# Performance work log

Measured on AMD Instinct MI355X. Metric: run time of the kernel, lower is better.

The kernel has to match this reference:

```python
import jax, jax.numpy as jnp
import numpy as np

E, H, FF, L, S, B = 64, 4, 32, 9, 7, 8192
HD = E // H


def setup_inputs() -> dict:
    key = jax.random.key(0)
    ks = iter(jax.random.split(key, 32))
    def rn(shape, scale=0.05):
        return jax.random.normal(next(ks), shape, dtype=jnp.float32) * scale
    inp = {
        "feature1": jax.random.normal(next(ks), (B, S, E), dtype=jnp.float32),
        "feature2": jax.random.normal(next(ks), (B, S, E), dtype=jnp.float32),
        # branch dim 2: index 0 = rotation, 1 = translation; then layer dim L
        "sa1_win": rn((2, L, 3 * E, E)), "sa1_bin": rn((2, L, 3 * E)),
        "sa1_wout": rn((2, L, E, E)), "sa1_bout": rn((2, L, E)),
        "sa2_win": rn((2, L, 3 * E, E)), "sa2_bin": rn((2, L, 3 * E)),
        "sa2_wout": rn((2, L, E, E)), "sa2_bout": rn((2, L, E)),
        "ca_win": rn((2, L, 3 * E, E)), "ca_bin": rn((2, L, 3 * E)),
        "ca_wout": rn((2, L, E, E)), "ca_bout": rn((2, L, E)),
        "ff_w1": rn((2, L, FF, E)), "ff_b1": rn((2, L, FF)),
        "ff_w2": rn((2, L, E, FF)), "ff_b2": rn((2, L, E)),
        "query_embed": jax.random.normal(next(ks), (2, S, E), dtype=jnp.float32),
        "fc_rot_w": rn((4, E)), "fc_rot_b": rn((4,)),
        "fc_trans_w": rn((3, E)), "fc_trans_b": rn((3,)),
    }
    return inp


def mha(q_in, kv_in, win, b_in, wout, bout):
    # torch nn.MultiheadAttention with batch_first=True
    wq, wk, wv = win[:E], win[E:2 * E], win[2 * E:]
    bq, bk, bv = b_in[:E], b_in[E:2 * E], b_in[2 * E:]
    b, sq, _ = q_in.shape
    sk = kv_in.shape[1]
    q = (q_in @ wq.T + bq).reshape(b, sq, H, HD)
    k = (kv_in @ wk.T + bk).reshape(b, sk, H, HD)
    v = (kv_in @ wv.T + bv).reshape(b, sk, H, HD)
    scores = jnp.einsum("bqhd,bkhd->bhqk", q, k) / jnp.sqrt(jnp.float32(HD))
    attn = jax.nn.softmax(scores, axis=-1)
    ctx = jnp.einsum("bhqk,bkhd->bqhd", attn, v).reshape(b, sq, E)
    return ctx @ wout.T + bout


def _branch(f1, f2, query, bi, sa1_win, sa1_bin, sa1_wout, sa1_bout,
            sa2_win, sa2_bin, sa2_wout, sa2_bout,
            ca_win, ca_bin, ca_wout, ca_bout, ff_w1, ff_b1, ff_w2, ff_b2):
    q = query
    for i in range(L):
        f1 = f1 + mha(f1, f1, sa1_win[bi, i], sa1_bin[bi, i], sa1_wout[bi, i], sa1_bout[bi, i])
        f2 = f2 + mha(f2, f2, sa2_win[bi, i], sa2_bin[bi, i], sa2_wout[bi, i], sa2_bout[bi, i])
        kv = jnp.concatenate([f1, f2], axis=1)  # (B, 2S, E)
        q = q + mha(q, kv, ca_win[bi, i], ca_bin[bi, i], ca_wout[bi, i], ca_bout[bi, i])
        h = jax.nn.relu(q @ ff_w1[bi, i].T + ff_b1[bi, i])
        q = q + h @ ff_w2[bi, i].T + ff_b2[bi, i]
    return q


def reference(feature1, feature2, sa1_win, sa1_bin, sa1_wout, sa1_bout,
              sa2_win, sa2_bin, sa2_wout, sa2_bout,
              ca_win, ca_bin, ca_wout, ca_bout,
              ff_w1, ff_b1, ff_w2, ff_b2, query_embed,
              fc_rot_w, fc_rot_b, fc_trans_w, fc_trans_b):
    b = feature1.shape[0]
    args = (sa1_win, sa1_bin, sa1_wout, sa1_bout, sa2_win, sa2_bin, sa2_wout,
            sa2_bout, ca_win, ca_bin, ca_wout, ca_bout, ff_w1, ff_b1, ff_w2, ff_b2)
    q_rot = jnp.broadcast_to(query_embed[0][None], (b, S, E))
    q_trn = jnp.broadcast_to(query_embed[1][None], (b, S, E))
    # rotation and translation branches are mathematically independent
    rot = _branch(feature1, feature2, q_rot, 0, *args)
    trn = _branch(feature1, feature2, q_trn, 1, *args)
    pose_rot = (rot @ fc_rot_w.T + fc_rot_b).mean(axis=1)    # (B, 4)
    pose_trn = (trn @ fc_trans_w.T + fc_trans_b).mean(axis=1)  # (B, 3)
    return jnp.concatenate([pose_rot, pose_trn], axis=1)  # (B, 7)
```

## Files before the change

kernel.cpp:

```cpp
#include <hip/hip_runtime.h>
#include <hip/hip_bf16.h>

namespace {

using bf16x8 = __attribute__((ext_vector_type(8))) short;
using f32x4  = __attribute__((ext_vector_type(4))) float;

constexpr int NL = 9, S = 7, BB = 8192;
constexpr int G = 8;
constexpr int M = G * S;
constexpr int NT = 512;

constexpr int OFF_F1 = 0;
constexpr int OFF_F2 = 14336;
constexpr int OFF_Q  = 28672;
constexpr int OFF_QB = 43008;
constexpr int OFF_KB = 50176;
constexpr int OFF_VT = 64512;
constexpr int SMEM_TOTAL = 80896;

__device__ __forceinline__ unsigned short f2bf(float f) {
  union { __hip_bfloat16 h; unsigned short s; } u;
  u.h = __float2bfloat16(f);
  return u.s;
}
__device__ __forceinline__ uint32_t pk2(float a, float b) {
  return (uint32_t)f2bf(a) | ((uint32_t)f2bf(b) << 16);
}
__device__ __forceinline__ int swzS(int r, int c) {
  return r * 256 + ((((c >> 3) ^ (r & 7)) << 5) | ((c & 7) << 2));
}
__device__ __forceinline__ int swzB(int r, int c) {
  return r * 128 + ((((c >> 3) ^ (r & 7)) << 4) | ((c & 7) << 1));
}
__device__ __forceinline__ int swzV(int d, int kv) {
  return d * 256 + ((((kv >> 3) ^ (d & 7)) << 4) | ((kv & 7) << 1));
}
__device__ __forceinline__ int div7(int t) { return (t * 9363) >> 16; }

__device__ __forceinline__ bf16x8 ldStateFrag(const char* base, int r, int k0) {
  const float4* p = (const float4*)(base + r * 256 + (((k0 >> 3) ^ (r & 7)) << 5));
  float4 x = p[0], y = p[1];
  union { bf16x8 v; uint32_t u[4]; } o;
  o.u[0] = pk2(x.x, x.y); o.u[1] = pk2(x.z, x.w);
  o.u[2] = pk2(y.x, y.y); o.u[3] = pk2(y.z, y.w);
  return o.v;
}
__device__ __forceinline__ bf16x8 ldBfFrag(const char* base, int r, int k0) {
  return *(const bf16x8*)(base + r * 128 + (((k0 >> 3) ^ (r & 7)) << 4));
}

template <int MTOT, int NTOT, int KF, int WMG, int WNG, int VNT, bool WS,
          class BLD, class STN, class STV>
__device__ __forceinline__ void gemm_sw(const short* __restrict__ wbf,
                                        const float* __restrict__ wf,
                                        const float* __restrict__ bias,
                                        int ldK, int wid, int lane,
                                        BLD bld, STN stn, STV stv)
{
  const int wm = wid / WNG, wn = wid % WNG;
  const int q = lane & 15, gI = lane >> 4;
  constexpr int MPW = (MTOT + WMG - 1) / WMG;
  constexpr int NPW = NTOT / WNG;
  bf16x8 bfr[MPW][KF];
#pragma unroll
  for (int i = 0; i < MPW; ++i) {
    const int mt = wm * MPW + i;
    if (mt < MTOT) {
#pragma unroll
      for (int kf = 0; kf < KF; ++kf)
        bfr[i][kf] = bld(mt * 16 + q, kf * 32 + gI * 8);
    }
  }
#pragma unroll
  for (int j = 0; j < NPW; ++j) {
    const int nt = wn * NPW + j;
    bf16x8 afr[KF];
#pragma unroll
    for (int kf = 0; kf < KF; ++kf) {
      const int k0 = kf * 32 + gI * 8;
      if constexpr (WS) {
        afr[kf] = *(const bf16x8*)(wbf + (size_t)(nt * 16 + q) * ldK + k0);
      } else {
        const float* wp = wf + (size_t)(nt * 16 + q) * ldK + k0;
        float4 x = *(const float4*)wp, y = *(const float4*)(wp + 4);
        union { bf16x8 v; uint32_t u[4]; } o;
        o.u[0] = pk2(x.x, x.y); o.u[1] = pk2(x.z, x.w);
        o.u[2] = pk2(y.x, y.y); o.u[3] = pk2(y.z, y.w);
        afr[kf] = o.v;
      }
    }
    if (nt < VNT) {
      const float4 b4 = *(const float4*)(bias + nt * 16 + gI * 4);
#pragma unroll
      for (int i = 0; i < MPW; ++i) {
        const int mt = wm * MPW + i;
        if (mt < MTOT) {
          f32x4 acc = { b4.x, b4.y, b4.z, b4.w };
#pragma unroll
          for (int kf = 0; kf < KF; ++kf)
            acc = __builtin_amdgcn_mfma_f32_16x16x32_bf16(afr[kf], bfr[i][kf], acc, 0, 0, 0);
          stn(mt, nt, acc);
        }
      }
    } else {
      const float bv = bias[nt * 16 + q];
#pragma unroll
      for (int i = 0; i < MPW; ++i) {
        const int mt = wm * MPW + i;
        if (mt < MTOT) {
          f32x4 acc = { bv, bv, bv, bv };
#pragma unroll
          for (int kf = 0; kf < KF; ++kf)
            acc = __builtin_amdgcn_mfma_f32_16x16x32_bf16(bfr[i][kf], afr[kf], acc, 0, 0, 0);
          stv(mt, nt, acc);
        }
      }
    }
  }
}

template <bool CA_>
__device__ __forceinline__ void attn(char* qb, const char* kb, const char* vt,
                                     int wid, int lane)
{
  const int q = lane & 15, gI = lane >> 4;
  const int g = wid;
  constexpr int KVL = CA_ ? 14 : 7;
#pragma unroll
  for (int h = 0; h < 4; ++h) {
    bf16x8 kfrag = {}, qfrag = {};
    if (gI < 2) {
      int qrow = g * 7 + q; qrow = qrow > 55 ? 55 : qrow;
      qfrag = ldBfFrag(qb, qrow, h * 16 + gI * 8);
      int kvr;
      if constexpr (CA_) {
        kvr = (q < 7) ? (g * 7 + q) : (49 + g * 7 + q);
        kvr = kvr > 111 ? 111 : kvr;
      } else {
        kvr = g * 7 + q; kvr = kvr > 55 ? 55 : kvr;
      }
      kfrag = ldBfFrag(kb, kvr, h * 16 + gI * 8);
    }
    f32x4 s = { 0.f, 0.f, 0.f, 0.f };
    s = __builtin_amdgcn_mfma_f32_16x16x32_bf16(kfrag, qfrag, s, 0, 0, 0);

    float e[4]; float sum = 0.f;
#pragma unroll
    for (int jj = 0; jj < 4; ++jj) {
      const int kvloc = gI * 4 + jj;
      const float tt = fminf(s[jj] * 0.36067376f, 60.f);
      e[jj] = (kvloc < KVL) ? exp2f(tt) : 0.f;
      sum += e[jj];
    }
    sum += __shfl_xor(sum, 16);
    sum += __shfl_xor(sum, 32);
    const float inv = __builtin_amdgcn_rcpf(sum);

    union { bf16x8 v; uint32_t u[4]; } pb;
    pb.u[0] = pk2(e[0] * inv, e[1] * inv);
    pb.u[1] = pk2(e[2] * inv, e[3] * inv);
    pb.u[2] = 0; pb.u[3] = 0;

    const int d = h * 16 + q;
    const int kv0 = (CA_ ? g * 16 : g * 8) + gI * 4;
    const uint2 vv = *(const uint2*)(vt + swzV(d, kv0));
    union { bf16x8 v; uint32_t u[4]; } va;
    va.u[0] = vv.x; va.u[1] = vv.y; va.u[2] = 0; va.u[3] = 0;

    f32x4 o = { 0.f, 0.f, 0.f, 0.f };
    o = __builtin_amdgcn_mfma_f32_16x16x32_bf16(va.v, pb.v, o, 0, 0, 0);

    if (q < 7) {
      const int tok = g * 7 + q, c0 = h * 16 + gI * 4;
      *(uint2*)(qb + swzB(tok, c0)) = make_uint2(pk2(o[0], o[1]), pk2(o[2], o[3]));
    }
  }
}

template <bool WS>
__global__ __launch_bounds__(NT, 4) void pose_kernel(
    const float* __restrict__ feature1, const float* __restrict__ feature2,
    const float* __restrict__ sa1_win, const float* __restrict__ sa1_bin,
    const float* __restrict__ sa1_wout, const float* __restrict__ sa1_bout,
    const float* __restrict__ sa2_win, const float* __restrict__ sa2_bin,
    const float* __restrict__ sa2_wout, const float* __restrict__ sa2_bout,
    const float* __restrict__ ca_win, const float* __restrict__ ca_bin,
    const float* __restrict__ ca_wout, const float* __restrict__ ca_bout,
    const float* __restrict__ ff_w1, const float* __restrict__ ff_b1,
    const float* __restrict__ ff_w2, const float* __restrict__ ff_b2,
    const float* __restrict__ query_embed,
    const float* __restrict__ fc_rot_w, const float* __restrict__ fc_rot_b,
    const float* __restrict__ fc_trans_w, const float* __restrict__ fc_trans_b,
    const short* __restrict__ wbf, float* __restrict__ out)
{
  extern __shared__ char smem[];
  char* sF1 = smem + OFF_F1;
  char* sF2 = smem + OFF_F2;
  char* sQ  = smem + OFF_Q;
  char* qb  = smem + OFF_QB;
  char* kb  = smem + OFF_KB;
  char* vt  = smem + OFF_VT;

  const int t = threadIdx.x;
  const int wid = t >> 6, lane = t & 63;
  const int q = lane & 15, gI = lane >> 4;
  const int bi = blockIdx.y;
  const int b0 = blockIdx.x * G;

  {
    const uint4 z = { 0, 0, 0, 0 };
    for (int i = t; i < 1024; i += NT) ((uint4*)vt)[i] = z;
  }
  {
    const float* f1p = feature1 + (size_t)b0 * (S * 64);
    const float* f2p = feature2 + (size_t)b0 * (S * 64);
    const float* qe  = query_embed + (size_t)bi * (S * 64);
    for (int idx = t; idx < M * 64; idx += NT) {
      const int r = idx >> 6, c = idx & 63;
      const int s = r - div7(r) * 7;
      *(float*)(sF1 + swzS(r, c)) = f1p[idx];
      *(float*)(sF2 + swzS(r, c)) = f2p[idx];
      *(float*)(sQ + swzS(r, c))  = qe[s * 64 + c];
    }
  }
  __syncthreads();

  const auto stv_none = [](int, int, f32x4) {};

  for (int li = 0; li < NL; ++li) {
    const int wo = bi * NL + li;
    const short* W_in[3]  = { wbf + 0      + wo * 12288,
                              wbf + 221184 + wo * 12288,
                              wbf + 442368 + wo * 12288 };
    const short* W_out[3] = { wbf + 663552 + wo * 4096,
                              wbf + 737280 + wo * 4096,
                              wbf + 811008 + wo * 4096 };
    const short* W_f1 = wbf + 884736 + wo * 2048;
    const short* W_f2 = wbf + 921600 + wo * 2048;
    const float* F_in[3]  = { sa1_win + wo * 12288, sa2_win + wo * 12288, ca_win + wo * 12288 };
    const float* F_out[3] = { sa1_wout + wo * 4096, sa2_wout + wo * 4096, ca_wout + wo * 4096 };
    const float* B_in[3]  = { sa1_bin + wo * 192, sa2_bin + wo * 192, ca_bin + wo * 192 };
    const float* B_out[3] = { sa1_bout + wo * 64, sa2_bout + wo * 64, ca_bout + wo * 64 };

    for (int sa = 0; sa < 2; ++sa) {
      char* ST = sa ? sF2 : sF1;
      auto bld = [&](int r, int k0) { return ldStateFrag(ST, r > 55 ? 55 : r, k0); };
      auto stn = [&](int mt, int nt, f32x4 a) {
        const int tok = mt * 16 + q; if (tok >= M) return;
        if (nt < 4) {
          *(uint2*)(qb + swzB(tok, nt * 16 + gI * 4)) =
              make_uint2(pk2(a[0], a[1]), pk2(a[2], a[3]));
        } else {
          *(uint2*)(kb + swzB(tok, (nt - 4) * 16 + gI * 4)) =
              make_uint2(pk2(a[0], a[1]), pk2(a[2], a[3]));
        }
      };
      auto stv = [&](int mt, int nt, f32x4 a) {
        const int d = (nt - 8) * 16 + q;
#pragma unroll
        for (int jj = 0; jj < 4; ++jj) {
          const int tok = mt * 16 + gI * 4 + jj;
          if (tok < M) {
            const int g = div7(tok);
            *(short*)(vt + swzV(d, g * 8 + (tok - g * 7))) = (short)f2bf(a[jj]);
          }
        }
      };
      gemm_sw<4, 12, 2, 2, 4, 8, WS>(W_in[sa], F_in[sa], B_in[sa], 64, wid, lane, bld, stn, stv);
      __syncthreads();
      attn<false>(qb, kb, vt, wid, lane);
      __syncthreads();
      auto bldc = [&](int r, int k0) { return ldBfFrag(qb, r > 55 ? 55 : r, k0); };
      auto stres = [&](int mt, int nt, f32x4 a) {
        const int tok = mt * 16 + q; if (tok >= M) return;
        const int c0 = nt * 16 + gI * 4;
        float4* p = (float4*)(ST + tok * 256 + (((c0 >> 3) ^ (tok & 7)) << 5) + (c0 & 7) * 4);
        float4 v = *p;
        v.x += a[0]; v.y += a[1]; v.z += a[2]; v.w += a[3];
        *p = v;
      };
      gemm_sw<4, 4, 2, 2, 4, 4, WS>(W_out[sa], F_out[sa], B_out[sa], 64, wid, lane, bldc, stres, stv_none);
      __syncthreads();
    }

    {
      auto bldq = [&](int r, int k0) { return ldStateFrag(sQ, r > 55 ? 55 : r, k0); };
      auto stq = [&](int mt, int nt, f32x4 a) {
        const int tok = mt * 16 + q; if (tok >= M) return;
        *(uint2*)(qb + swzB(tok, nt * 16 + gI * 4)) =
            make_uint2(pk2(a[0], a[1]), pk2(a[2], a[3]));
      };
      gemm_sw<4, 4, 2, 2, 4, 4, WS>(W_in[2], F_in[2], B_in[2], 64, wid, lane, bldq, stq, stv_none);

      for (int src = 0; src < 2; ++src) {
        const char* SRC = src ? sF2 : sF1;
        auto bld = [&](int r, int k0) { return ldStateFrag(SRC, r > 55 ? 55 : r, k0); };
        auto stk = [&](int mt, int nt, f32x4 a) {
          const int tok = mt * 16 + q; if (tok >= M) return;
          *(uint2*)(kb + swzB(tok + src * 56, nt * 16 + gI * 4)) =
              make_uint2(pk2(a[0], a[1]), pk2(a[2], a[3]));
        };
        auto stv = [&](int mt, int nt, f32x4 a) {
          const int d = (nt - 4) * 16 + q;
#pragma unroll
          for (int jj = 0; jj < 4; ++jj) {
            const int tok = mt * 16 + gI * 4 + jj;
            if (tok < M) {
              const int g = div7(tok);
              *(short*)(vt + swzV(d, g * 16 + (tok - g * 7) + src * 7)) = (short)f2bf(a[jj]);
            }
          }
        };
        gemm_sw<4, 8, 2, 2, 4, 4, WS>(W_in[2] + 4096, F_in[2] + 4096, B_in[2] + 64,
                                      64, wid, lane, bld, stk, stv);
      }
      __syncthreads();
      attn<true>(qb, kb, vt, wid, lane);
      __syncthreads();
      auto bldc = [&](int r, int k0) { return ldBfFrag(qb, r > 55 ? 55 : r, k0); };
      auto stres = [&](int mt, int nt, f32x4 a) {
        const int tok = mt * 16 + q; if (tok >= M) return;
        const int c0 = nt * 16 + gI * 4;
        float4* p = (float4*)(sQ + tok * 256 + (((c0 >> 3) ^ (tok & 7)) << 5) + (c0 & 7) * 4);
        float4 v = *p;
        v.x += a[0]; v.y += a[1]; v.z += a[2]; v.w += a[3];
        *p = v;
      };
      gemm_sw<4, 4, 2, 2, 4, 4, WS>(W_out[2], F_out[2], B_out[2], 64, wid, lane, bldc, stres, stv_none);
      __syncthreads();
    }

    {
      auto bldq = [&](int r, int k0) { return ldStateFrag(sQ, r > 55 ? 55 : r, k0); };
      auto sth = [&](int mt, int nt, f32x4 a) {
        const int tok = mt * 16 + q; if (tok >= M) return;
        *(uint2*)(qb + swzB(tok, nt * 16 + gI * 4)) =
            make_uint2(pk2(fmaxf(a[0], 0.f), fmaxf(a[1], 0.f)),
                       pk2(fmaxf(a[2], 0.f), fmaxf(a[3], 0.f)));
      };
      gemm_sw<4, 2, 2, 4, 2, 2, WS>(W_f1, ff_w1 + wo * 2048, ff_b1 + wo * 32,
                                    64, wid, lane, bldq, sth, stv_none);
      __syncthreads();
      auto bldh = [&](int r, int k0) { return ldBfFrag(qb, r > 55 ? 55 : r, k0); };
      auto stres = [&](int mt, int nt, f32x4 a) {
        const int tok = mt * 16 + q; if (tok >= M) return;
        const int c0 = nt * 16 + gI * 4;
        float4* p = (float4*)(sQ + tok * 256 + (((c0 >> 3) ^ (tok & 7)) << 5) + (c0 & 7) * 4);
        float4 v = *p;
        v.x += a[0]; v.y += a[1]; v.z += a[2]; v.w += a[3];
        *p = v;
      };
      gemm_sw<4, 4, 1, 2, 4, 4, WS>(W_f2, ff_w2 + wo * 2048, ff_b2 + wo * 64,
                                    32, wid, lane, bldh, stres, stv_none);
      __syncthreads();
    }
  }

  float* cs = (float*)qb;
  {
    const int g = t >> 6, c = t & 63;
    float a = 0.f;
#pragma unroll
    for (int s = 0; s < 7; ++s) a += *(const float*)(sQ + swzS(g * 7 + s, c));
    cs[t] = a;
  }
  __syncthreads();
  const int ncols = bi ? 3 : 4;
  if (t < G * ncols) {
    const int g = t / ncols, cc = t - g * ncols;
    const float* wv = bi ? (fc_trans_w + cc * 64) : (fc_rot_w + cc * 64);
    float acc = 0.f;
#pragma unroll
    for (int k = 0; k < 64; ++k) acc += cs[g * 64 + k] * wv[k];
    const float bb = bi ? fc_trans_b[cc] : fc_rot_b[cc];
    out[(size_t)(b0 + g) * 7 + (bi ? 4 : 0) + cc] = acc * (1.f / 7.f) + bb;
  }
}

__global__ void prep_kernel(const float* __restrict__ a0, const float* __restrict__ a1,
                            const float* __restrict__ a2, const float* __restrict__ a3,
                            const float* __restrict__ a4, const float* __restrict__ a5,
                            const float* __restrict__ a6, const float* __restrict__ a7,
                            short* __restrict__ dst)
{
  for (int i = blockIdx.x * blockDim.x + threadIdx.x; i < 958464;
       i += gridDim.x * blockDim.x) {
    const float* s; int j;
    if      (i < 221184) { s = a0; j = i; }
    else if (i < 442368) { s = a1; j = i - 221184; }
    else if (i < 663552) { s = a2; j = i - 442368; }
    else if (i < 737280) { s = a3; j = i - 663552; }
    else if (i < 811008) { s = a4; j = i - 737280; }
    else if (i < 884736) { s = a5; j = i - 811008; }
    else if (i < 921600) { s = a6; j = i - 884736; }
    else                 { s = a7; j = i - 921600; }
    dst[i] = (short)f2bf(s[j]);
  }
}

}

extern "C" void kernel_launch(void* const* d_in, const int* in_sizes, int n_in,
                              void* d_out, int out_size, void* d_ws, size_t ws_size,
                              hipStream_t stream)
{
  const float* feature1    = (const float*)d_in[0];
  const float* feature2    = (const float*)d_in[1];
  const float* sa1_win     = (const float*)d_in[2];
  const float* sa1_bin     = (const float*)d_in[3];
  const float* sa1_wout    = (const float*)d_in[4];
  const float* sa1_bout    = (const float*)d_in[5];
  const float* sa2_win     = (const float*)d_in[6];
  const float* sa2_bin     = (const float*)d_in[7];
  const float* sa2_wout    = (const float*)d_in[8];
  const float* sa2_bout    = (const float*)d_in[9];
  const float* ca_win      = (const float*)d_in[10];
  const float* ca_bin      = (const float*)d_in[11];
  const float* ca_wout     = (const float*)d_in[12];
  const float* ca_bout     = (const float*)d_in[13];
  const float* ff_w1       = (const float*)d_in[14];
  const float* ff_b1       = (const float*)d_in[15];
  const float* ff_w2       = (const float*)d_in[16];
  const float* ff_b2       = (const float*)d_in[17];
  const float* query_embed = (const float*)d_in[18];
  const float* fc_rot_w    = (const float*)d_in[19];
  const float* fc_rot_b    = (const float*)d_in[20];
  const float* fc_trans_w  = (const float*)d_in[21];
  const float* fc_trans_b  = (const float*)d_in[22];

  const bool ws_ok = (d_ws != nullptr) && (ws_size >= (size_t)958464 * 2);
  dim3 grid(BB / G, 2);

  if (ws_ok) {
    prep_kernel<<<dim3(936), 512, 0, stream>>>(sa1_win, sa2_win, ca_win,
                                               sa1_wout, sa2_wout, ca_wout,
                                               ff_w1, ff_w2, (short*)d_ws);
    hipFuncSetAttribute(reinterpret_cast<const void*>(&pose_kernel<true>),
                        hipFuncAttributeMaxDynamicSharedMemorySize, SMEM_TOTAL);
    pose_kernel<true><<<grid, NT, SMEM_TOTAL, stream>>>(
        feature1, feature2,
        sa1_win, sa1_bin, sa1_wout, sa1_bout,
        sa2_win, sa2_bin, sa2_wout, sa2_bout,
        ca_win, ca_bin, ca_wout, ca_bout,
        ff_w1, ff_b1, ff_w2, ff_b2,
        query_embed, fc_rot_w, fc_rot_b, fc_trans_w, fc_trans_b,
        (const short*)d_ws, (float*)d_out);
  } else {
    hipFuncSetAttribute(reinterpret_cast<const void*>(&pose_kernel<false>),
                        hipFuncAttributeMaxDynamicSharedMemorySize, SMEM_TOTAL);
    pose_kernel<false><<<grid, NT, SMEM_TOTAL, stream>>>(
        feature1, feature2,
        sa1_win, sa1_bin, sa1_wout, sa1_bout,
        sa2_win, sa2_bin, sa2_wout, sa2_bout,
        ca_win, ca_bin, ca_wout, ca_bout,
        ff_w1, ff_b1, ff_w2, ff_b2,
        query_embed, fc_rot_w, fc_rot_b, fc_trans_w, fc_trans_b,
        (const short*)d_ws, (float*)d_out);
  }
}
```

Before: 1.301 ms.

## Pack 7 batches per block and merge self-attention stages to cut padding and barriers

Reduces the batch group per block from 8 to 7 so that 49 tokens pack tightly into 4 MFMA row tiles, down from 56 tokens, cutting wasted padding. Both self-attention branches now share one synchronisation phase: QKV projections run back to back, a single attention pass spreads 14 units over 8 waves, and the two output projections run together. The CA K/V projection handles F1 and F2 in one 98-row GEMM. Per-layer barriers drop, but the grid needs a partial last block with bounds checks, and the attention load across waves is uneven.

```diff
diff --git a/kernel.cpp b/kernel.cpp
--- a/kernel.cpp
+++ b/kernel.cpp
@@ -6,18 +6,18 @@
 using bf16x8 = __attribute__((ext_vector_type(8))) short;
 using f32x4  = __attribute__((ext_vector_type(4))) float;
 
-constexpr int NL = 9, S = 7, BB = 8192;
-constexpr int G = 8;
-constexpr int M = G * S;
+constexpr int NL = 9, BB = 8192;
+constexpr int G = 7;
+constexpr int M1 = 49;
 constexpr int NT = 512;
 
 constexpr int OFF_F1 = 0;
-constexpr int OFF_F2 = 14336;
-constexpr int OFF_Q  = 28672;
-constexpr int OFF_QB = 43008;
+constexpr int OFF_F2 = 12544;
+constexpr int OFF_SQ = 25088;
+constexpr int OFF_QB = 37632;
 constexpr int OFF_KB = 50176;
-constexpr int OFF_VT = 64512;
-constexpr int SMEM_TOTAL = 80896;
+constexpr int OFF_VT = 62720;
+constexpr int SMEM_TOTAL = 79104;
 
 __device__ __forceinline__ unsigned short f2bf(float f) {
   union { __hip_bfloat16 h; unsigned short s; } u;
@@ -50,26 +50,107 @@
   return *(const bf16x8*)(base + r * 128 + (((k0 >> 3) ^ (r & 7)) << 4));
 }
 
-template <int MTOT, int NTOT, int KF, int WMG, int WNG, int VNT, bool WS,
-          class BLD, class STN, class STV>
-__device__ __forceinline__ void gemm_sw(const short* __restrict__ wbf,
-                                        const float* __restrict__ wf,
-                                        const float* __restrict__ bias,
-                                        int ldK, int wid, int lane,
-                                        BLD bld, STN stn, STV stv)
+enum : int { BS_F1 = 0, BS_F2, BS_SQ, BS_F1F2, BS_QB0, BS_QB49 };
+
+template <int BS>
+__device__ __forceinline__ bf16x8 bfrag(const char* smem, int r, int k0)
+{
+  if constexpr (BS == BS_F1) {
+    return ldStateFrag(smem + OFF_F1, r > 48 ? 48 : r, k0);
+  } else if constexpr (BS == BS_F2) {
+    return ldStateFrag(smem + OFF_F2, r > 48 ? 48 : r, k0);
+  } else if constexpr (BS == BS_SQ) {
+    return ldStateFrag(smem + OFF_SQ, r > 48 ? 48 : r, k0);
+  } else if constexpr (BS == BS_F1F2) {
+    const int f2 = r >= 49;
+    int rr = f2 ? r - 49 : r;
+    rr = rr > 48 ? 48 : rr;
+    return ldStateFrag(smem + (f2 ? OFF_F2 : OFF_F1), rr, k0);
+  } else if constexpr (BS == BS_QB0) {
+    return ldBfFrag(smem + OFF_QB, r > 97 ? 97 : r, k0);
+  } else {
+    int rr = r > 48 ? 48 : r;
+    return ldBfFrag(smem + OFF_QB, 49 + rr, k0);
+  }
+}
+
+enum : int { OM_QKV0 = 0, OM_QKV1, OM_QCA, OM_KVCA, OM_RESF0, OM_RESF1, OM_RESQ, OM_RELU };
+
+template <int OM>
+__device__ __forceinline__ void epi_n(char* smem, int nt, int tok, int gI, f32x4 a)
+{
+  if constexpr (OM == OM_RESF0 || OM == OM_RESF1 || OM == OM_RESQ) {
+    constexpr int off = (OM == OM_RESF0) ? OFF_F1 : (OM == OM_RESF1) ? OFF_F2 : OFF_SQ;
+    const int c0 = nt * 16 + gI * 4;
+    float4* p = (float4*)(smem + off + tok * 256 + (((c0 >> 3) ^ (tok & 7)) << 5) + ((c0 & 7) << 2));
+    float4 v = *p;
+    v.x += a[0]; v.y += a[1]; v.z += a[2]; v.w += a[3];
+    *p = v;
+  } else if constexpr (OM == OM_RELU) {
+    *(uint2*)(smem + OFF_QB + swzB(tok, nt * 16 + gI * 4)) =
+        make_uint2(pk2(fmaxf(a[0], 0.f), fmaxf(a[1], 0.f)),
+                   pk2(fmaxf(a[2], 0.f), fmaxf(a[3], 0.f)));
+  } else {
+    const uint2 val = make_uint2(pk2(a[0], a[1]), pk2(a[2], a[3]));
+    if constexpr (OM == OM_QKV0 || OM == OM_QKV1) {
+      constexpr int RO = (OM == OM_QKV1) ? 49 : 0;
+      if (nt < 4) *(uint2*)(smem + OFF_QB + swzB(RO + tok, nt * 16 + gI * 4)) = val;
+      else        *(uint2*)(smem + OFF_KB + swzB(RO + tok, (nt - 4) * 16 + gI * 4)) = val;
+    } else if constexpr (OM == OM_QCA) {
+      *(uint2*)(smem + OFF_QB + swzB(tok, nt * 16 + gI * 4)) = val;
+    } else {
+      const int f2 = tok >= 49;
+      const int t2 = f2 ? tok - 49 : tok;
+      const int g = div7(t2);
+      const int row = 14 * g + (t2 - 7 * g) + (f2 ? 7 : 0);
+      *(uint2*)(smem + OFF_KB + swzB(row, nt * 16 + gI * 4)) = val;
+    }
+  }
+}
+
+template <int OM>
+__device__ __forceinline__ void epi_v(char* smem, int d, int tokbase, f32x4 a)
+{
+#pragma unroll
+  for (int jj = 0; jj < 4; ++jj) {
+    const int tok = tokbase + jj;
+    if constexpr (OM == OM_QKV0 || OM == OM_QKV1) {
+      if (tok < 49) {
+        const int g = div7(tok);
+        const int slot = ((OM == OM_QKV1) ? 56 : 0) + 8 * g + (tok - 7 * g);
+        *(short*)(smem + OFF_VT + swzV(d, slot)) = (short)f2bf(a[jj]);
+      }
+    } else {
+      if (tok < 98) {
+        const int f2 = tok >= 49;
+        const int t2 = f2 ? tok - 49 : tok;
+        const int g = div7(t2);
+        const int slot = 16 * g + (t2 - 7 * g) + (f2 ? 7 : 0);
+        *(short*)(smem + OFF_VT + swzV(d, slot)) = (short)f2bf(a[jj]);
+      }
+    }
+  }
+}
+
+template <int MTI, int MV, int NTOT, int KF, int WMG, int WNG, int VNT,
+          int BS, int OM, int NBOFF, int VBOFF, int LDK, bool WS>
+__device__ __forceinline__ void gemm(char* smem, const short* __restrict__ wbf,
+                                     const float* __restrict__ wf,
+                                     const float* __restrict__ bias,
+                                     int wid, int lane)
 {
   const int wm = wid / WNG, wn = wid % WNG;
   const int q = lane & 15, gI = lane >> 4;
-  constexpr int MPW = (MTOT + WMG - 1) / WMG;
+  constexpr int MPW = (MTI + WMG - 1) / WMG;
   constexpr int NPW = NTOT / WNG;
   bf16x8 bfr[MPW][KF];
 #pragma unroll
   for (int i = 0; i < MPW; ++i) {
     const int mt = wm * MPW + i;
-    if (mt < MTOT) {
+    if (mt < MTI) {
 #pragma unroll
       for (int kf = 0; kf < KF; ++kf)
-        bfr[i][kf] = bld(mt * 16 + q, kf * 32 + gI * 8);
+        bfr[i][kf] = bfrag<BS>(smem, mt * 16 + q, kf * 32 + gI * 8);
     }
   }
 #pragma unroll
@@ -80,9 +161,9 @@
     for (int kf = 0; kf < KF; ++kf) {
       const int k0 = kf * 32 + gI * 8;
       if constexpr (WS) {
-        afr[kf] = *(const bf16x8*)(wbf + (size_t)(nt * 16 + q) * ldK + k0);
+        afr[kf] = *(const bf16x8*)(wbf + (nt * 16 + q) * LDK + k0);
       } else {
-        const float* wp = wf + (size_t)(nt * 16 + q) * ldK + k0;
+        const float* wp = wf + (nt * 16 + q) * LDK + k0;
         float4 x = *(const float4*)wp, y = *(const float4*)(wp + 4);
         union { bf16x8 v; uint32_t u[4]; } o;
         o.u[0] = pk2(x.x, x.y); o.u[1] = pk2(x.z, x.w);
@@ -91,80 +172,78 @@
       }
     }
     if (nt < VNT) {
-      const float4 b4 = *(const float4*)(bias + nt * 16 + gI * 4);
+      const float4 b4 = *(const float4*)(bias + NBOFF + nt * 16 + gI * 4);
 #pragma unroll
       for (int i = 0; i < MPW; ++i) {
         const int mt = wm * MPW + i;
-        if (mt < MTOT) {
+        if (mt < MTI) {
           f32x4 acc = { b4.x, b4.y, b4.z, b4.w };
 #pragma unroll
           for (int kf = 0; kf < KF; ++kf)
             acc = __builtin_amdgcn_mfma_f32_16x16x32_bf16(afr[kf], bfr[i][kf], acc, 0, 0, 0);
-          stn(mt, nt, acc);
+          const int tok = mt * 16 + q;
+          if (tok < MV) epi_n<OM>(smem, nt, tok, gI, acc);
         }
       }
     } else {
-      const float bv = bias[nt * 16 + q];
+      const float bv = bias[VBOFF + (nt - VNT) * 16 + q];
 #pragma unroll
       for (int i = 0; i < MPW; ++i) {
         const int mt = wm * MPW + i;
-        if (mt < MTOT) {
+        if (mt < MTI) {
           f32x4 acc = { bv, bv, bv, bv };
 #pragma unroll
           for (int kf = 0; kf < KF; ++kf)
             acc = __builtin_amdgcn_mfma_f32_16x16x32_bf16(bfr[i][kf], afr[kf], acc, 0, 0, 0);
-          stv(mt, nt, acc);
+          epi_v<OM>(smem, (nt - VNT) * 16 + q, mt * 16 + gI * 4, acc);
         }
       }
     }
   }
 }
 
-template <bool CA_>
-__device__ __forceinline__ void attn(char* qb, const char* kb, const char* vt,
-                                     int wid, int lane)
+__device__ __forceinline__ void attn_unit(char* smem, int qrow0, int krow0,
+                                          int cb, int kvl, int lane)
 {
   const int q = lane & 15, gI = lane >> 4;
-  const int g = wid;
-  constexpr int KVL = CA_ ? 14 : 7;
+  char* qb = smem + OFF_QB;
+  const char* kb = smem + OFF_KB;
+  const char* vt = smem + OFF_VT;
 #pragma unroll
   for (int h = 0; h < 4; ++h) {
     bf16x8 kfrag = {}, qfrag = {};
     if (gI < 2) {
-      int qrow = g * 7 + q; qrow = qrow > 55 ? 55 : qrow;
-      qfrag = ldBfFrag(qb, qrow, h * 16 + gI * 8);
-      int kvr;
-      if constexpr (CA_) {
-        kvr = (q < 7) ? (g * 7 + q) : (49 + g * 7 + q);
-        kvr = kvr > 111 ? 111 : kvr;
-      } else {
-        kvr = g * 7 + q; kvr = kvr > 55 ? 55 : kvr;
-      }
-      kfrag = ldBfFrag(kb, kvr, h * 16 + gI * 8);
+      const int qr = qrow0 + (q < 7 ? q : 6);
+      qfrag = ldBfFrag(qb, qr, h * 16 + gI * 8);
+      const int kr = krow0 + (q < kvl ? q : kvl - 1);
+      kfrag = ldBfFrag(kb, kr, h * 16 + gI * 8);
     }
     f32x4 s = { 0.f, 0.f, 0.f, 0.f };
     s = __builtin_amdgcn_mfma_f32_16x16x32_bf16(kfrag, qfrag, s, 0, 0, 0);
 
-    float e[4]; float sum = 0.f;
-#pragma unroll
-    for (int jj = 0; jj < 4; ++jj) {
-      const int kvloc = gI * 4 + jj;
-      const float tt = fminf(s[jj] * 0.36067376f, 60.f);
-      e[jj] = (kvloc < KVL) ? exp2f(tt) : 0.f;
-      sum += e[jj];
+    float e0, e1, e2, e3; float sum;
+    {
+      const float t0 = fminf(s[0] * 0.36067376f, 60.f);
+      const float t1 = fminf(s[1] * 0.36067376f, 60.f);
+      const float t2 = fminf(s[2] * 0.36067376f, 60.f);
+      const float t3 = fminf(s[3] * 0.36067376f, 60.f);
+      e0 = (gI * 4 + 0 < kvl) ? exp2f(t0) : 0.f;
+      e1 = (gI * 4 + 1 < kvl) ? exp2f(t1) : 0.f;
+      e2 = (gI * 4 + 2 < kvl) ? exp2f(t2) : 0.f;
+      e3 = (gI * 4 + 3 < kvl) ? exp2f(t3) : 0.f;
+      sum = e0 + e1 + e2 + e3;
     }
     sum += __shfl_xor(sum, 16);
     sum += __shfl_xor(sum, 32);
     const float inv = __builtin_amdgcn_rcpf(sum);
 
     union { bf16x8 v; uint32_t u[4]; } pb;
-    pb.u[0] = pk2(e[0] * inv, e[1] * inv);
-    pb.u[1] = pk2(e[2] * inv, e[3] * inv);
+    pb.u[0] = pk2(e0 * inv, e1 * inv);
+    pb.u[1] = pk2(e2 * inv, e3 * inv);
     pb.u[2] = 0; pb.u[3] = 0;
 
     const int d = h * 16 + q;
-    const int kv0 = (CA_ ? g * 16 : g * 8) + gI * 4;
-    const uint2 vv = *(const uint2*)(vt + swzV(d, kv0));
+    const uint2 vv = *(const uint2*)(vt + swzV(d, cb + gI * 4));
     union { bf16x8 v; uint32_t u[4]; } va;
     va.u[0] = vv.x; va.u[1] = vv.y; va.u[2] = 0; va.u[3] = 0;
 
@@ -172,8 +251,8 @@
     o = __builtin_amdgcn_mfma_f32_16x16x32_bf16(va.v, pb.v, o, 0, 0, 0);
 
     if (q < 7) {
-      const int tok = g * 7 + q, c0 = h * 16 + gI * 4;
-      *(uint2*)(qb + swzB(tok, c0)) = make_uint2(pk2(o[0], o[1]), pk2(o[2], o[3]));
+      *(uint2*)(qb + swzB(qrow0 + q, h * 16 + gI * 4)) =
+          make_uint2(pk2(o[0], o[1]), pk2(o[2], o[3]));
     }
   }
 }
@@ -195,186 +274,102 @@
     const short* __restrict__ wbf, float* __restrict__ out)
 {
   extern __shared__ char smem[];
-  char* sF1 = smem + OFF_F1;
-  char* sF2 = smem + OFF_F2;
-  char* sQ  = smem + OFF_Q;
-  char* qb  = smem + OFF_QB;
-  char* kb  = smem + OFF_KB;
-  char* vt  = smem + OFF_VT;
-
   const int t = threadIdx.x;
   const int wid = t >> 6, lane = t & 63;
-  const int q = lane & 15, gI = lane >> 4;
   const int bi = blockIdx.y;
   const int b0 = blockIdx.x * G;
 
   {
     const uint4 z = { 0, 0, 0, 0 };
-    for (int i = t; i < 1024; i += NT) ((uint4*)vt)[i] = z;
+    for (int i = t; i < 1024; i += NT) ((uint4*)(smem + OFF_VT))[i] = z;
   }
   {
-    const float* f1p = feature1 + (size_t)b0 * (S * 64);
-    const float* f2p = feature2 + (size_t)b0 * (S * 64);
-    const float* qe  = query_embed + (size_t)bi * (S * 64);
-    for (int idx = t; idx < M * 64; idx += NT) {
+    const float* f1p = feature1 + (size_t)b0 * 448;
+    const float* f2p = feature2 + (size_t)b0 * 448;
+    const float* qe  = query_embed + (size_t)bi * 448;
+    const int lim = (BB - b0) * 448;
+    for (int idx = t; idx < M1 * 64; idx += NT) {
       const int r = idx >> 6, c = idx & 63;
       const int s = r - div7(r) * 7;
-      *(float*)(sF1 + swzS(r, c)) = f1p[idx];
-      *(float*)(sF2 + swzS(r, c)) = f2p[idx];
-      *(float*)(sQ + swzS(r, c))  = qe[s * 64 + c];
+      const bool ok = idx < lim;
+      *(float*)(smem + OFF_F1 + swzS(r, c)) = ok ? f1p[idx] : 0.f;
+      *(float*)(smem + OFF_F2 + swzS(r, c)) = ok ? f2p[idx] : 0.f;
+      *(float*)(smem + OFF_SQ + swzS(r, c)) = qe[s * 64 + c];
     }
   }
   __syncthreads();
-
-  const auto stv_none = [](int, int, f32x4) {};
 
   for (int li = 0; li < NL; ++li) {
     const int wo = bi * NL + li;
-    const short* W_in[3]  = { wbf + 0      + wo * 12288,
-                              wbf + 221184 + wo * 12288,
-                              wbf + 442368 + wo * 12288 };
-    const short* W_out[3] = { wbf + 663552 + wo * 4096,
-                              wbf + 737280 + wo * 4096,
-                              wbf + 811008 + wo * 4096 };
-    const short* W_f1 = wbf + 884736 + wo * 2048;
-    const short* W_f2 = wbf + 921600 + wo * 2048;
-    const float* F_in[3]  = { sa1_win + wo * 12288, sa2_win + wo * 12288, ca_win + wo * 12288 };
-    const float* F_out[3] = { sa1_wout + wo * 4096, sa2_wout + wo * 4096, ca_wout + wo * 4096 };
-    const float* B_in[3]  = { sa1_bin + wo * 192, sa2_bin + wo * 192, ca_bin + wo * 192 };
-    const float* B_out[3] = { sa1_bout + wo * 64, sa2_bout + wo * 64, ca_bout + wo * 64 };
-
-    for (int sa = 0; sa < 2; ++sa) {
-      char* ST = sa ? sF2 : sF1;
-      auto bld = [&](int r, int k0) { return ldStateFrag(ST, r > 55 ? 55 : r, k0); };
-      auto stn = [&](int mt, int nt, f32x4 a) {
-        const int tok = mt * 16 + q; if (tok >= M) return;
-        if (nt < 4) {
-          *(uint2*)(qb + swzB(tok, nt * 16 + gI * 4)) =
-              make_uint2(pk2(a[0], a[1]), pk2(a[2], a[3]));
-        } else {
-          *(uint2*)(kb + swzB(tok, (nt - 4) * 16 + gI * 4)) =
-              make_uint2(pk2(a[0], a[1]), pk2(a[2], a[3]));
-        }
-      };
-      auto stv = [&](int mt, int nt, f32x4 a) {
-        const int d = (nt - 8) * 16 + q;
-#pragma unroll
-        for (int jj = 0; jj < 4; ++jj) {
-          const int tok = mt * 16 + gI * 4 + jj;
-          if (tok < M) {
-            const int g = div7(tok);
-            *(short*)(vt + swzV(d, g * 8 + (tok - g * 7))) = (short)f2bf(a[jj]);
-          }
-        }
-      };
-      gemm_sw<4, 12, 2, 2, 4, 8, WS>(W_in[sa], F_in[sa], B_in[sa], 64, wid, lane, bld, stn, stv);
-      __syncthreads();
-      attn<false>(qb, kb, vt, wid, lane);
-      __syncthreads();
-      auto bldc = [&](int r, int k0) { return ldBfFrag(qb, r > 55 ? 55 : r, k0); };
-      auto stres = [&](int mt, int nt, f32x4 a) {
-        const int tok = mt * 16 + q; if (tok >= M) return;
-        const int c0 = nt * 16 + gI * 4;
-        float4* p = (float4*)(ST + tok * 256 + (((c0 >> 3) ^ (tok & 7)) << 5) + (c0 & 7) * 4);
-        float4 v = *p;
-        v.x += a[0]; v.y += a[1]; v.z += a[2]; v.w += a[3];
-        *p = v;
-      };
-      gemm_sw<4, 4, 2, 2, 4, 4, WS>(W_out[sa], F_out[sa], B_out[sa], 64, wid, lane, bldc, stres, stv_none);
-      __syncthreads();
-    }
+
+    gemm<4, 49, 12, 2, 2, 4, 8, BS_F1, OM_QKV0, 0, 128, 64, WS>(
+        smem, wbf + wo * 12288, sa1_win + wo * 12288, sa1_bin + wo * 192, wid, lane);
+    gemm<4, 49, 12, 2, 2, 4, 8, BS_F2, OM_QKV1, 0, 128, 64, WS>(
+        smem, wbf + 221184 + wo * 12288, sa2_win + wo * 12288, sa2_bin + wo * 192, wid, lane);
+    __syncthreads();
 
     {
-      auto bldq = [&](int r, int k0) { return ldStateFrag(sQ, r > 55 ? 55 : r, k0); };
-      auto stq = [&](int mt, int nt, f32x4 a) {
-        const int tok = mt * 16 + q; if (tok >= M) return;
-        *(uint2*)(qb + swzB(tok, nt * 16 + gI * 4)) =
-            make_uint2(pk2(a[0], a[1]), pk2(a[2], a[3]));
-      };
-      gemm_sw<4, 4, 2, 2, 4, 4, WS>(W_in[2], F_in[2], B_in[2], 64, wid, lane, bldq, stq, stv_none);
-
-      for (int src = 0; src < 2; ++src) {
-        const char* SRC = src ? sF2 : sF1;
-        auto bld = [&](int r, int k0) { return ldStateFrag(SRC, r > 55 ? 55 : r, k0); };
-        auto stk = [&](int mt, int nt, f32x4 a) {
-          const int tok = mt * 16 + q; if (tok >= M) return;
-          *(uint2*)(kb + swzB(tok + src * 56, nt * 16 + gI * 4)) =
-              make_uint2(pk2(a[0], a[1]), pk2(a[2], a[3]));
-        };
-        auto stv = [&](int mt, int nt, f32x4 a) {
-          const int d = (nt - 4) * 16 + q;
-#pragma unroll
-          for (int jj = 0; jj < 4; ++jj) {
-            const int tok = mt * 16 + gI * 4 + jj;
-            if (tok < M) {
-              const int g = div7(tok);
-              *(short*)(vt + swzV(d, g * 16 + (tok - g * 7) + src * 7)) = (short)f2bf(a[jj]);
-            }
-          }
-        };
-        gemm_sw<4, 8, 2, 2, 4, 4, WS>(W_in[2] + 4096, F_in[2] + 4096, B_in[2] + 64,
-                                      64, wid, lane, bld, stk, stv);
-      }
-      __syncthreads();
-      attn<true>(qb, kb, vt, wid, lane);
-      __syncthreads();
-      auto bldc = [&](int r, int k0) { return ldBfFrag(qb, r > 55 ? 55 : r, k0); };
-      auto stres = [&](int mt, int nt, f32x4 a) {
-        const int tok = mt * 16 + q; if (tok >= M) return;
-        const int c0 = nt * 16 + gI * 4;
-        float4* p = (float4*)(sQ + tok * 256 + (((c0 >> 3) ^ (tok & 7)) << 5) + (c0 & 7) * 4);
-        float4 v = *p;
-        v.x += a[0]; v.y += a[1]; v.z += a[2]; v.w += a[3];
-        *p = v;
-      };
-      gemm_sw<4, 4, 2, 2, 4, 4, WS>(W_out[2], F_out[2], B_out[2], 64, wid, lane, bldc, stres, stv_none);
-      __syncthreads();
-    }
-
-    {
-      auto bldq = [&](int r, int k0) { return ldStateFrag(sQ, r > 55 ? 55 : r, k0); };
-      auto sth = [&](int mt, int nt, f32x4 a) {
-        const int tok = mt * 16 + q; if (tok >= M) return;
-        *(uint2*)(qb + swzB(tok, nt * 16 + gI * 4)) =
-            make_uint2(pk2(fmaxf(a[0], 0.f), fmaxf(a[1], 0.f)),
-                       pk2(fmaxf(a[2], 0.f), fmaxf(a[3], 0.f)));
-      };
-      gemm_sw<4, 2, 2, 4, 2, 2, WS>(W_f1, ff_w1 + wo * 2048, ff_b1 + wo * 32,
-                                    64, wid, lane, bldq, sth, stv_none);
-      __syncthreads();
-      auto bldh = [&](int r, int k0) { return ldBfFrag(qb, r > 55 ? 55 : r, k0); };
-      auto stres = [&](int mt, int nt, f32x4 a) {
-        const int tok = mt * 16 + q; if (tok >= M) return;
-        const int c0 = nt * 16 + gI * 4;
-        float4* p = (float4*)(sQ + tok * 256 + (((c0 >> 3) ^ (tok & 7)) << 5) + (c0 & 7) * 4);
-        float4 v = *p;
-        v.x += a[0]; v.y += a[1]; v.z += a[2]; v.w += a[3];
-        *p = v;
-      };
-      gemm_sw<4, 4, 1, 2, 4, 4, WS>(W_f2, ff_w2 + wo * 2048, ff_b2 + wo * 64,
-                                    32, wid, lane, bldh, stres, stv_none);
-      __syncthreads();
-    }
-  }
-
-  float* cs = (float*)qb;
-  {
+      const int u = wid;
+      const int sa = u >= 7, g = u - 7 * sa;
+      attn_unit(smem, 49 * sa + 7 * g, 49 * sa + 7 * g, 56 * sa + 8 * g, 7, lane);
+      const int u2 = wid + 8;
+      if (u2 < 14) {
+        const int g2 = u2 - 7;
+        attn_unit(smem, 49 + 7 * g2, 49 + 7 * g2, 56 + 8 * g2, 7, lane);
+      }
+    }
+    __syncthreads();
+
+    gemm<4, 49, 4, 2, 2, 4, 99, BS_QB0, OM_RESF0, 0, 0, 64, WS>(
+        smem, wbf + 663552 + wo * 4096, sa1_wout + wo * 4096, sa1_bout + wo * 64, wid, lane);
+    gemm<4, 49, 4, 2, 2, 4, 99, BS_QB49, OM_RESF1, 0, 0, 64, WS>(
+        smem, wbf + 737280 + wo * 4096, sa2_wout + wo * 4096, sa2_bout + wo * 64, wid, lane);
+    __syncthreads();
+
+    gemm<4, 49, 4, 2, 2, 4, 99, BS_SQ, OM_QCA, 0, 0, 64, WS>(
+        smem, wbf + 442368 + wo * 12288, ca_win + wo * 12288, ca_bin + wo * 192, wid, lane);
+    gemm<7, 98, 8, 2, 2, 4, 4, BS_F1F2, OM_KVCA, 64, 128, 64, WS>(
+        smem, wbf + 442368 + wo * 12288 + 4096, ca_win + wo * 12288 + 4096,
+        ca_bin + wo * 192, wid, lane);
+    __syncthreads();
+
+    if (wid < 7)
+      attn_unit(smem, 7 * wid, 14 * wid, 16 * wid, 14, lane);
+    __syncthreads();
+
+    gemm<4, 49, 4, 2, 2, 4, 99, BS_QB0, OM_RESQ, 0, 0, 64, WS>(
+        smem, wbf + 811008 + wo * 4096, ca_wout + wo * 4096, ca_bout + wo * 64, wid, lane);
+    __syncthreads();
+
+    gemm<4, 49, 2, 2, 4, 2, 99, BS_SQ, OM_RELU, 0, 0, 64, WS>(
+        smem, wbf + 884736 + wo * 2048, ff_w1 + wo * 2048, ff_b1 + wo * 32, wid, lane);
+    __syncthreads();
+
+    gemm<4, 49, 4, 1, 2, 4, 99, BS_QB0, OM_RESQ, 0, 0, 32, WS>(
+        smem, wbf + 921600 + wo * 2048, ff_w2 + wo * 2048, ff_b2 + wo * 64, wid, lane);
+    __syncthreads();
+  }
+
+  float* cs = (float*)(smem + OFF_QB);
+  if (t < G * 64) {
     const int g = t >> 6, c = t & 63;
     float a = 0.f;
 #pragma unroll
-    for (int s = 0; s < 7; ++s) a += *(const float*)(sQ + swzS(g * 7 + s, c));
+    for (int s = 0; s < 7; ++s) a += *(const float*)(smem + OFF_SQ + swzS(g * 7 + s, c));
     cs[t] = a;
   }
   __syncthreads();
   const int ncols = bi ? 3 : 4;
   if (t < G * ncols) {
     const int g = t / ncols, cc = t - g * ncols;
-    const float* wv = bi ? (fc_trans_w + cc * 64) : (fc_rot_w + cc * 64);
-    float acc = 0.f;
-#pragma unroll
-    for (int k = 0; k < 64; ++k) acc += cs[g * 64 + k] * wv[k];
-    const float bb = bi ? fc_trans_b[cc] : fc_rot_b[cc];
-    out[(size_t)(b0 + g) * 7 + (bi ? 4 : 0) + cc] = acc * (1.f / 7.f) + bb;
+    if (b0 + g < BB) {
+      const float* wv = bi ? (fc_trans_w + cc * 64) : (fc_rot_w + cc * 64);
+      float acc = 0.f;
+#pragma unroll
+      for (int k = 0; k < 64; ++k) acc += cs[g * 64 + k] * wv[k];
+      const float bb = bi ? fc_trans_b[cc] : fc_rot_b[cc];
+      out[(size_t)(b0 + g) * 7 + (bi ? 4 : 0) + cc] = acc * (1.f / 7.f) + bb;
+    }
   }
 }
 
@@ -430,7 +425,7 @@
   const float* fc_trans_b  = (const float*)d_in[22];
 
   const bool ws_ok = (d_ws != nullptr) && (ws_size >= (size_t)958464 * 2);
-  dim3 grid(BB / G, 2);
+  dim3 grid((BB + G - 1) / G, 2);
 
   if (ws_ok) {
     prep_kernel<<<dim3(936), 512, 0, stream>>>(sa1_win, sa2_win, ca_win,
```

Measured after the change: 2.224 ms. 71.0% more time.
